# Optimization experiments

Hardware: AMD Instinct MI355X
Metric: run time of the kernel (lower is better)

Reference implementation:

```python
import jax, jax.numpy as jnp
import numpy as np

N_NODES = 50000
N_EDGES = 800000
HIDDEN = 128
BN_EPS = 1e-5
LEAKY_SLOPE = 0.01


def setup_inputs() -> dict:
    key = jax.random.key(0)
    ks = jax.random.split(key, 8)
    x = jax.random.normal(ks[0], (N_NODES, HIDDEN), dtype=jnp.float32)
    edge_index = jax.random.randint(ks[1], (2, N_EDGES), 0, N_NODES, dtype=jnp.int64)
    # stacked per-layer params (4 SAGEConv layers, all 128->128)
    sc = 1.0 / np.sqrt(HIDDEN)
    Wl = jax.random.normal(ks[2], (4, HIDDEN, HIDDEN), dtype=jnp.float32) * sc
    bl = jax.random.normal(ks[3], (4, HIDDEN), dtype=jnp.float32) * sc
    Wr = jax.random.normal(ks[4], (4, HIDDEN, HIDDEN), dtype=jnp.float32) * sc
    gamma = jnp.ones((4, HIDDEN), dtype=jnp.float32)
    beta = jnp.zeros((4, HIDDEN), dtype=jnp.float32)
    return {"x": x, "edge_index": edge_index, "Wl": Wl, "bl": bl,
            "Wr": Wr, "gamma": gamma, "beta": beta}


def _sage_mean_agg(x, src, dst, n):
    # gather source features per edge, scatter-mean onto destination nodes
    msg = x[src]                                                  # [E, F]
    agg = jax.ops.segment_sum(msg, dst, num_segments=n)           # [N, F]
    cnt = jax.ops.segment_sum(jnp.ones_like(dst, dtype=x.dtype), dst, num_segments=n)
    return agg / jnp.maximum(cnt, 1.0)[:, None]


def _bn_train(x, g, b):
    mu = jnp.mean(x, axis=0)
    var = jnp.mean((x - mu) ** 2, axis=0)  # biased variance (PyTorch BN normalization)
    return (x - mu) * jax.lax.rsqrt(var + BN_EPS) * g + b


def reference(x, edge_index, Wl, bl, Wr, gamma, beta):
    src, dst = edge_index[0], edge_index[1]
    n = x.shape[0]
    h = x
    for i in range(4):
        agg = _sage_mean_agg(h, src, dst, n)
        h = agg @ Wl[i] + bl[i] + h @ Wr[i]          # SAGEConv: lin_l(mean_nbr) + lin_r(root)
        h = jnp.where(h >= 0, h, LEAKY_SLOPE * h)    # leaky_relu
        h = _bn_train(h, gamma[i], beta[i])
    # dropout: eval-mode identity (deterministic reference)
    return h
```

## Files before the change

### kernel.cpp

```cpp
#include <hip/hip_runtime.h>
#include <hip/hip_bf16.h>

#define N_NODES 50000
#define N_EDGES 800000
#define F 128
#define BN_EPS 1e-5f
#define SLOPE 0.01f
#define NB 782
#define CAP 64
#define NBIN 128
#define BINSZ 391
#define QCAP2 8192
#define ABLK 512
#define AITER 7
#define PB1 6250
#define PB2 512

typedef __attribute__((ext_vector_type(8))) __bf16 bf16x8_t;
typedef __attribute__((ext_vector_type(8))) unsigned short u16x8_t;
typedef __attribute__((ext_vector_type(4))) float f32x4_t;

__device__ __forceinline__ unsigned short f2b(float f) {
    unsigned int u = __float_as_uint(f);
    unsigned int r = (u + 0x7fffu + ((u >> 16) & 1u)) >> 16;
    return (unsigned short)r;
}
__device__ __forceinline__ float b2f_lo(unsigned int v) { return __uint_as_float(v << 16); }
__device__ __forceinline__ float b2f_hi(unsigned int v) { return __uint_as_float(v & 0xffff0000u); }


__global__ __launch_bounds__(256) void bucket2_kernel(const int* __restrict__ src,
                                                      const int* __restrict__ dst,
                                                      int* __restrict__ qtail,
                                                      unsigned int* __restrict__ qdata) {
    __shared__ int counts[NBIN];
    __shared__ int cur[NBIN];
    __shared__ int base[NBIN];
    const int tid = threadIdx.x;

    for (int k = tid; k < NBIN; k += 256) { counts[k] = 0; cur[k] = 0; }
    __syncthreads();

    unsigned int pack[AITER];
    int bin[AITER];
    const int stride = ABLK * 256;
#pragma unroll
    for (int it = 0; it < AITER; ++it) {
        const int e = blockIdx.x * 256 + tid + it * stride;
        bin[it] = -1;
        if (e < N_EDGES) {
            int d = __builtin_nontemporal_load(dst + e);
            int s = __builtin_nontemporal_load(src + e);
            bin[it] = d / BINSZ;
            pack[it] = ((unsigned int)d << 16) | (unsigned int)s;
            atomicAdd(&counts[bin[it]], 1);
        }
    }
    __syncthreads();
    if (tid < NBIN) {
        int c = counts[tid];
        base[tid] = (c > 0) ? atomicAdd(&qtail[tid * 16], c) : 0;
    }
    __syncthreads();
#pragma unroll
    for (int it = 0; it < AITER; ++it) {
        if (bin[it] >= 0) {
            int slot = base[bin[it]] + atomicAdd(&cur[bin[it]], 1);
            qdata[(long)bin[it] * QCAP2 + slot] = pack[it];
        }
    }
}

__global__ __launch_bounds__(256) void scatter2_kernel(const unsigned int* __restrict__ qdata,
                                                       const int* __restrict__ qtail,
                                                       int* __restrict__ deg,
                                                       unsigned short* __restrict__ csr) {
    __shared__ int cnt[BINSZ];
    __shared__ unsigned short stage[BINSZ][CAP];
    const int b = blockIdx.x;
    const int nbase = b * BINSZ;
    const int nn = min(BINSZ, N_NODES - nbase);
    const int tid = threadIdx.x;

    for (int r = tid; r < BINSZ; r += 256) cnt[r] = 0;
    __syncthreads();

    const int n = qtail[b * 16];
    const unsigned int* q = qdata + (long)b * QCAP2;
    for (int i = tid; i < n; i += 256) {
        unsigned int p = q[i];
        int local = (int)(p >> 16) - nbase;
        int pos = atomicAdd(&cnt[local], 1);
        if (pos < CAP) stage[local][pos] = (unsigned short)(p & 0xffff);
    }
    __syncthreads();

    for (int c = tid; c < nn * (CAP / 8); c += 256) {
        const int r = c >> 3;
        const int col = (c & 7) * 8;
        *(u16x8_t*)(csr + (long)(nbase + r) * CAP + col) = *(const u16x8_t*)&stage[r][col];
    }
    for (int r = tid; r < nn; r += 256) deg[nbase + r] = min(cnt[r], CAP);
}


__global__ __launch_bounds__(256) void prep_kernel(const float* __restrict__ x,
                                                   unsigned short* __restrict__ hb,
                                                   const float* __restrict__ Wl,
                                                   const float* __restrict__ Wr,
                                                   unsigned short* __restrict__ Wt,
                                                   float* __restrict__ scale,
                                                   float* __restrict__ shift) {
    const int b = blockIdx.x;
    const int tid = threadIdx.x;
    if (b < PB1) {
        long i = (long)b * 256 + tid;
        float4 v = ((const float4*)x)[i];
        ushort4 o;
        o.x = f2b(v.x); o.y = f2b(v.y); o.z = f2b(v.z); o.w = f2b(v.w);
        ((ushort4*)hb)[i] = o;
    } else if (b < PB1 + PB2) {
        int idx = (b - PB1) * 256 + tid;
        int k = idx & 255;
        int n = (idx >> 8) & 127;
        int i = idx >> 15;
        float v = (k < F) ? Wl[((long)i * F + k) * F + n]
                          : Wr[((long)i * F + (k - F)) * F + n];
        Wt[idx] = f2b(v);
    } else {
        if (tid < F) { scale[tid] = 1.f; shift[tid] = 0.f; }
    }
}


__global__ __launch_bounds__(256) void agg_kernel(const unsigned short* __restrict__ h,
                                                  const int* __restrict__ deg,
                                                  const unsigned short* __restrict__ csr,
                                                  const float* __restrict__ scale,
                                                  const float* __restrict__ shift,
                                                  unsigned short* __restrict__ agg) {
    int node = (int)((blockIdx.x * (unsigned)blockDim.x + threadIdx.x) >> 6);
    int lane = threadIdx.x & 63;
    if (node >= N_NODES) return;
    const int g = lane >> 4;
    const int fl = lane & 15;
    const int d = deg[node];
    const int beg = node * CAP;
    const unsigned short* hl = h + fl * 8;

    float a0 = 0.f, a1 = 0.f, a2 = 0.f, a3 = 0.f;
    float a4 = 0.f, a5 = 0.f, a6 = 0.f, a7 = 0.f;

    for (int e0 = 0; e0 < d; e0 += 16) {
        int idx[4];
#pragma unroll
        for (int s = 0; s < 4; ++s) {
            const int ee = e0 + s * 4 + g;
            idx[s] = (int)csr[beg + ((ee < d) ? ee : 0)];
        }
        uint4 v[4];
#pragma unroll
        for (int s = 0; s < 4; ++s)
            v[s] = *(const uint4*)(hl + (long)idx[s] * F);
#pragma unroll
        for (int s = 0; s < 4; ++s) {
            const bool ok = (e0 + s * 4 + g) < d;
            const unsigned int w0 = ok ? v[s].x : 0u;
            const unsigned int w1 = ok ? v[s].y : 0u;
            const unsigned int w2 = ok ? v[s].z : 0u;
            const unsigned int w3 = ok ? v[s].w : 0u;
            a0 += b2f_lo(w0); a1 += b2f_hi(w0);
            a2 += b2f_lo(w1); a3 += b2f_hi(w1);
            a4 += b2f_lo(w2); a5 += b2f_hi(w2);
            a6 += b2f_lo(w3); a7 += b2f_hi(w3);
        }
    }

    a0 += __shfl_xor(a0, 16); a1 += __shfl_xor(a1, 16);
    a2 += __shfl_xor(a2, 16); a3 += __shfl_xor(a3, 16);
    a4 += __shfl_xor(a4, 16); a5 += __shfl_xor(a5, 16);
    a6 += __shfl_xor(a6, 16); a7 += __shfl_xor(a7, 16);
    a0 += __shfl_xor(a0, 32); a1 += __shfl_xor(a1, 32);
    a2 += __shfl_xor(a2, 32); a3 += __shfl_xor(a3, 32);
    a4 += __shfl_xor(a4, 32); a5 += __shfl_xor(a5, 32);
    a6 += __shfl_xor(a6, 32); a7 += __shfl_xor(a7, 32);

    u16x8_t o;
    if (d > 0) {
        const float inv = 1.0f / (float)d;
        const float4 sc0 = ((const float4*)scale)[fl * 2];
        const float4 sc1 = ((const float4*)scale)[fl * 2 + 1];
        const float4 sh0 = ((const float4*)shift)[fl * 2];
        const float4 sh1 = ((const float4*)shift)[fl * 2 + 1];
        o[0] = f2b(a0 * inv * sc0.x + sh0.x);
        o[1] = f2b(a1 * inv * sc0.y + sh0.y);
        o[2] = f2b(a2 * inv * sc0.z + sh0.z);
        o[3] = f2b(a3 * inv * sc0.w + sh0.w);
        o[4] = f2b(a4 * inv * sc1.x + sh1.x);
        o[5] = f2b(a5 * inv * sc1.y + sh1.y);
        o[6] = f2b(a6 * inv * sc1.z + sh1.z);
        o[7] = f2b(a7 * inv * sc1.w + sh1.w);
    } else {
#pragma unroll
        for (int j = 0; j < 8; ++j) o[j] = 0;
    }
    if (lane < 16)
        *(u16x8_t*)(agg + (long)node * F + lane * 8) = o;
}

__device__ __forceinline__ u16x8_t affine8(u16x8_t av, const float* __restrict__ sc,
                                           const float* __restrict__ sh) {
    u16x8_t r;
#pragma unroll
    for (int j = 0; j < 8; ++j) {
        float v = __uint_as_float(((unsigned int)av[j]) << 16);
        v = v * sc[j] + sh[j];
        r[j] = f2b(v);
    }
    return r;
}

__global__ __launch_bounds__(256) void gemm_mfma(const unsigned short* __restrict__ aggb,
                                                 const unsigned short* __restrict__ hin,
                                                 const float* __restrict__ scale,
                                                 const float* __restrict__ shift,
                                                 const unsigned short* __restrict__ Wt,
                                                 const float* __restrict__ bl,
                                                 unsigned short* __restrict__ Pb,
                                                 float* __restrict__ partial) {
    __shared__ __align__(16) char shraw[32768];
    unsigned short* stage = (unsigned short*)shraw;
    unsigned short* ep16 = (unsigned short*)shraw;
    __shared__ float lsum[4][F];
    __shared__ float lsq[4][F];

    const int tid = threadIdx.x;
    const int wave = tid >> 6, lane = tid & 63;
    const int m = lane & 15, q = lane >> 4;
    const int rbase = blockIdx.x * 64 + wave * 16;
    const int arow = rbase + m;
    const bool aval = arow < N_NODES;
    const unsigned short* ap = aggb + (long)arow * F + q * 8;
    const unsigned short* hp = hin + (long)arow * F + q * 8;

    u16x8_t areg[8];
#pragma unroll
    for (int j = 0; j < 8; ++j) areg[j] = (u16x8_t)0;
    if (aval) {
#pragma unroll
        for (int j = 0; j < 4; ++j) areg[j] = *(const u16x8_t*)(ap + j * 32);
#pragma unroll
        for (int j = 0; j < 4; ++j) {
            u16x8_t raw = *(const u16x8_t*)(hp + j * 32);
            const int base = j * 32 + q * 8;
            areg[4 + j] = affine8(raw, scale + base, shift + base);
        }
    }

    f32x4_t acc[8];
#pragma unroll
    for (int nt = 0; nt < 8; ++nt) acc[nt] = (f32x4_t){0.f, 0.f, 0.f, 0.f};

    for (int half = 0; half < 2; ++half) {
        if (half) __syncthreads();
#pragma unroll
        for (int f = 0; f < 8; ++f) {
            const int fid = f * 256 + tid;
            const int lf = fid & 63;
            const int ksf = (fid >> 6) & 3;
            const int ntf = fid >> 8;
            const int n = ntf * 16 + (lf & 15);
            const int k = half * 128 + ksf * 32 + (lf >> 4) * 8;
            const unsigned short* gsrc = Wt + (long)n * 256 + k;
#if __has_builtin(__builtin_amdgcn_global_load_lds)
            unsigned short* lbase = stage + (f * 256 + wave * 64) * 8;
            __builtin_amdgcn_global_load_lds(
                (const __attribute__((address_space(1))) void*)gsrc,
                (__attribute__((address_space(3))) void*)lbase, 16, 0, 0);
#else
            *(u16x8_t*)(stage + fid * 8) = *(const u16x8_t*)gsrc;
#endif
        }
        __syncthreads();
#pragma unroll
        for (int ks = 0; ks < 4; ++ks) {
            bf16x8_t af = __builtin_bit_cast(bf16x8_t, areg[half * 4 + ks]);
#pragma unroll
            for (int nt = 0; nt < 8; ++nt) {
                u16x8_t bv = *(const u16x8_t*)(stage + ((nt * 4 + ks) * 64 + lane) * 8);
                bf16x8_t bf = __builtin_bit_cast(bf16x8_t, bv);
                acc[nt] = __builtin_amdgcn_mfma_f32_16x16x32_bf16(af, bf, acc[nt], 0, 0, 0);
            }
        }
    }

    __syncthreads();

    float cs[8], cq[8];
#pragma unroll
    for (int nt = 0; nt < 8; ++nt) {
        cs[nt] = 0.f; cq[nt] = 0.f;
        const int c = nt * 16 + m;
        const float b = bl[c];
#pragma unroll
        for (int r = 0; r < 4; ++r) {
            const int rl = wave * 16 + q * 4 + r;
            float v = acc[nt][r] + b;
            v = (v >= 0.f) ? v : SLOPE * v;
            ep16[rl * 136 + c] = f2b(v);
            if (rbase + q * 4 + r < N_NODES) {
                cs[nt] += v;
                cq[nt] += v * v;
            }
        }
    }

    {
        const int rq = lane >> 4;
        const int cc = (lane & 15) * 8;
#pragma unroll
        for (int r2 = 0; r2 < 4; ++r2) {
            const int rl = wave * 16 + rq * 4 + r2;
            const int grow = blockIdx.x * 64 + rl;
            if (grow < N_NODES)
                *(u16x8_t*)(Pb + (long)grow * F + cc) = *(const u16x8_t*)(ep16 + rl * 136 + cc);
        }
    }

#pragma unroll
    for (int nt = 0; nt < 8; ++nt) {
        cs[nt] += __shfl_xor(cs[nt], 16);
        cs[nt] += __shfl_xor(cs[nt], 32);
        cq[nt] += __shfl_xor(cq[nt], 16);
        cq[nt] += __shfl_xor(cq[nt], 32);
    }
    if (lane < 16) {
#pragma unroll
        for (int nt = 0; nt < 8; ++nt) {
            lsum[wave][nt * 16 + m] = cs[nt];
            lsq[wave][nt * 16 + m] = cq[nt];
        }
    }
    __syncthreads();
    if (tid < F) {
        float s = 0.f, s2 = 0.f;
#pragma unroll
        for (int w = 0; w < 4; ++w) {
            s += lsum[w][tid];
            s2 += lsq[w][tid];
        }
        partial[(long)blockIdx.x * 256 + tid] = s;
        partial[(long)blockIdx.x * 256 + 128 + tid] = s2;
    }
}

__global__ __launch_bounds__(256) void bn_reduce(const float* __restrict__ partial,
                                                 const float* __restrict__ gamma,
                                                 const float* __restrict__ beta,
                                                 float* __restrict__ scale,
                                                 float* __restrict__ shift) {
    const int j = blockIdx.x;
    const int t = threadIdx.x;
    const int lane = t & 63, wave = t >> 6;
    float s = 0.f, s2 = 0.f;
    for (int b = t; b < NB; b += 256) {
        s += partial[(long)b * 256 + j];
        s2 += partial[(long)b * 256 + 128 + j];
    }
#pragma unroll
    for (int off = 1; off < 64; off <<= 1) {
        s += __shfl_xor(s, off);
        s2 += __shfl_xor(s2, off);
    }
    __shared__ float ls[4], lq[4];
    if (lane == 0) { ls[wave] = s; lq[wave] = s2; }
    __syncthreads();
    if (t == 0) {
        float S = ls[0] + ls[1] + ls[2] + ls[3];
        float Q = lq[0] + lq[1] + lq[2] + lq[3];
        const float inv_n = 1.0f / (float)N_NODES;
        float mu = S * inv_n;
        float var = Q * inv_n - mu * mu;
        float scl = gamma[j] * rsqrtf(var + BN_EPS);
        scale[j] = scl;
        shift[j] = beta[j] - mu * scl;
    }
}

__global__ __launch_bounds__(256) void bn_apply_f(const unsigned short* __restrict__ Pb,
                                                  float* __restrict__ out,
                                                  const float* __restrict__ scale,
                                                  const float* __restrict__ shift) {
    long i = (long)blockIdx.x * blockDim.x + threadIdx.x;
    if (i >= (long)N_NODES * (F / 8)) return;
    const int c8 = (int)(i & 15);
    uint4 v = ((const uint4*)Pb)[i];
    const float4 sc0 = ((const float4*)scale)[c8 * 2];
    const float4 sc1 = ((const float4*)scale)[c8 * 2 + 1];
    const float4 sh0 = ((const float4*)shift)[c8 * 2];
    const float4 sh1 = ((const float4*)shift)[c8 * 2 + 1];
    float4 o0, o1;
    o0.x = b2f_lo(v.x) * sc0.x + sh0.x;
    o0.y = b2f_hi(v.x) * sc0.y + sh0.y;
    o0.z = b2f_lo(v.y) * sc0.z + sh0.z;
    o0.w = b2f_hi(v.y) * sc0.w + sh0.w;
    o1.x = b2f_lo(v.z) * sc1.x + sh1.x;
    o1.y = b2f_hi(v.z) * sc1.y + sh1.y;
    o1.z = b2f_lo(v.w) * sc1.z + sh1.z;
    o1.w = b2f_hi(v.w) * sc1.w + sh1.w;
    ((float4*)out)[i * 2] = o0;
    ((float4*)out)[i * 2 + 1] = o1;
}


extern "C" void kernel_launch(void* const* d_in, const int* in_sizes, int n_in,
                              void* d_out, int out_size, void* d_ws, size_t ws_size,
                              hipStream_t stream) {
    const float* x     = (const float*)d_in[0];
    const int*   ei    = (const int*)d_in[1];
    const float* Wl    = (const float*)d_in[2];
    const float* bl    = (const float*)d_in[3];
    const float* Wr    = (const float*)d_in[4];
    const float* gamma = (const float*)d_in[5];
    const float* beta  = (const float*)d_in[6];
    float* out = (float*)d_out;

    const int* src = ei;
    const int* dst = ei + N_EDGES;

    char* w = (char*)d_ws;
    auto alloc = [&](size_t bytes) -> char* {
        char* p = w;
        w += (bytes + 255) & ~(size_t)255;
        return p;
    };
    unsigned short* hbA   = (unsigned short*)alloc((size_t)N_NODES * F * 2);
    unsigned short* hbB   = (unsigned short*)alloc((size_t)N_NODES * F * 2);
    unsigned short* aggb  = (unsigned short*)alloc((size_t)N_NODES * F * 2);
    unsigned short* Wt    = (unsigned short*)alloc((size_t)4 * F * 256 * 2);
    int*   deg      = (int*)alloc((size_t)N_NODES * 4);
    int*   qtail    = (int*)alloc((size_t)NBIN * 16 * 4);
    unsigned int* qdata = (unsigned int*)alloc((size_t)NBIN * QCAP2 * 4);
    unsigned short* csr = (unsigned short*)alloc((size_t)N_NODES * CAP * 2);
    float* partial  = (float*)alloc((size_t)NB * 256 * 4);
    float* scale    = (float*)alloc(F * 4);
    float* shift    = (float*)alloc(F * 4);

    hipMemsetAsync(qtail, 0, (size_t)NBIN * 16 * 4, stream);

    bucket2_kernel<<<ABLK, 256, 0, stream>>>(src, dst, qtail, qdata);
    scatter2_kernel<<<NBIN, 256, 0, stream>>>(qdata, qtail, deg, csr);
    prep_kernel<<<PB1 + PB2 + 1, 256, 0, stream>>>(x, hbA, Wl, Wr, Wt, scale, shift);

    const int n8 = N_NODES * (F / 8);

    unsigned short* hin = hbA;
    unsigned short* hnext = hbB;
    for (int i = 0; i < 4; ++i) {
        agg_kernel<<<(N_NODES + 3) / 4, 256, 0, stream>>>(hin, deg, csr, scale, shift, aggb);

        gemm_mfma<<<NB, 256, 0, stream>>>(
            aggb, hin, scale, shift, Wt + (size_t)i * F * 256, bl + (size_t)i * F,
            hnext, partial);

        bn_reduce<<<F, 256, 0, stream>>>(partial, gamma + (size_t)i * F, beta + (size_t)i * F,
                                         scale, shift);

        unsigned short* t = hin; hin = hnext; hnext = t;
    }
    bn_apply_f<<<(n8 + 255) / 256, 256, 0, stream>>>(hin, out, scale, shift);
}
```

Before: 355.1 us.

## Fuse neighbor mean aggregation into the MFMA GEMM kernel

Removes the separate aggregation kernel and its bf16 agg buffer. The GEMM kernel now gathers neighbor rows itself, with each lane walking one node's CSR list and accumulating 32 features while the first weight half is staged into LDS. This saves a kernel launch and the write and read-back of the aggregate buffer in every layer. In exchange the gather becomes serial per node with only 782 blocks of 4 waves, so there is much less memory-level parallelism and the serial per-edge index chain may leave gather latency exposed.

After: 400.2 us. 12.7% more time.

```diff
diff --git a/kernel.cpp b/kernel.cpp
--- a/kernel.cpp
+++ b/kernel.cpp
@@ -133,101 +133,80 @@
 }
 
 
-__global__ __launch_bounds__(256) void agg_kernel(const unsigned short* __restrict__ h,
+__device__ __forceinline__ u16x8_t affine8(u16x8_t av, const float* __restrict__ sc,
+                                           const float* __restrict__ sh) {
+    u16x8_t r;
+#pragma unroll
+    for (int j = 0; j < 8; ++j) {
+        float v = __uint_as_float(((unsigned int)av[j]) << 16);
+        v = v * sc[j] + sh[j];
+        r[j] = f2b(v);
+    }
+    return r;
+}
+
+#define ACC8(A, V)                               \
+    A[0] += b2f_lo(V.x); A[1] += b2f_hi(V.x);    \
+    A[2] += b2f_lo(V.y); A[3] += b2f_hi(V.y);    \
+    A[4] += b2f_lo(V.z); A[5] += b2f_hi(V.z);    \
+    A[6] += b2f_lo(V.w); A[7] += b2f_hi(V.w);
+
+#define PACKJ(j, A) {                                                   \
+    const float4 s0 = *(const float4*)(scale + q * 8 + 32 * (j));       \
+    const float4 s1 = *(const float4*)(scale + q * 8 + 32 * (j) + 4);   \
+    const float4 t0 = *(const float4*)(shift + q * 8 + 32 * (j));       \
+    const float4 t1 = *(const float4*)(shift + q * 8 + 32 * (j) + 4);   \
+    u16x8_t r;                                                          \
+    r[0] = f2b(A[0] * inv * s0.x + t0.x);                               \
+    r[1] = f2b(A[1] * inv * s0.y + t0.y);                               \
+    r[2] = f2b(A[2] * inv * s0.z + t0.z);                               \
+    r[3] = f2b(A[3] * inv * s0.w + t0.w);                               \
+    r[4] = f2b(A[4] * inv * s1.x + t1.x);                               \
+    r[5] = f2b(A[5] * inv * s1.y + t1.y);                               \
+    r[6] = f2b(A[6] * inv * s1.z + t1.z);                               \
+    r[7] = f2b(A[7] * inv * s1.w + t1.w);                               \
+    areg[j] = r; }
+
+#if __has_builtin(__builtin_amdgcn_global_load_lds)
+#define STAGE_HALF(half) {                                                        \
+    _Pragma("unroll")                                                             \
+    for (int f = 0; f < 8; ++f) {                                                 \
+        const int fid = f * 256 + tid;                                            \
+        const int lf = fid & 63;                                                  \
+        const int ksf = (fid >> 6) & 3;                                           \
+        const int ntf = fid >> 8;                                                 \
+        const int n = ntf * 16 + (lf & 15);                                       \
+        const int k = (half) * 128 + ksf * 32 + (lf >> 4) * 8;                    \
+        const unsigned short* gsrc = Wt + (long)n * 256 + k;                      \
+        unsigned short* lbase = stage + (f * 256 + wave * 64) * 8;                \
+        __builtin_amdgcn_global_load_lds(                                         \
+            (const __attribute__((address_space(1))) void*)gsrc,                  \
+            (__attribute__((address_space(3))) void*)lbase, 16, 0, 0);            \
+    } }
+#else
+#define STAGE_HALF(half) {                                                        \
+    _Pragma("unroll")                                                             \
+    for (int f = 0; f < 8; ++f) {                                                 \
+        const int fid = f * 256 + tid;                                            \
+        const int lf = fid & 63;                                                  \
+        const int ksf = (fid >> 6) & 3;                                           \
+        const int ntf = fid >> 8;                                                 \
+        const int n = ntf * 16 + (lf & 15);                                       \
+        const int k = (half) * 128 + ksf * 32 + (lf >> 4) * 8;                    \
+        const unsigned short* gsrc = Wt + (long)n * 256 + k;                      \
+        *(u16x8_t*)(stage + fid * 8) = *(const u16x8_t*)gsrc;                     \
+    } }
+#endif
+
+__global__ __launch_bounds__(256) void gemm_fused(const unsigned short* __restrict__ hin,
                                                   const int* __restrict__ deg,
                                                   const unsigned short* __restrict__ csr,
                                                   const float* __restrict__ scale,
                                                   const float* __restrict__ shift,
-                                                  unsigned short* __restrict__ agg) {
-    int node = (int)((blockIdx.x * (unsigned)blockDim.x + threadIdx.x) >> 6);
-    int lane = threadIdx.x & 63;
-    if (node >= N_NODES) return;
-    const int g = lane >> 4;
-    const int fl = lane & 15;
-    const int d = deg[node];
-    const int beg = node * CAP;
-    const unsigned short* hl = h + fl * 8;
-
-    float a0 = 0.f, a1 = 0.f, a2 = 0.f, a3 = 0.f;
-    float a4 = 0.f, a5 = 0.f, a6 = 0.f, a7 = 0.f;
-
-    for (int e0 = 0; e0 < d; e0 += 16) {
-        int idx[4];
-#pragma unroll
-        for (int s = 0; s < 4; ++s) {
-            const int ee = e0 + s * 4 + g;
-            idx[s] = (int)csr[beg + ((ee < d) ? ee : 0)];
-        }
-        uint4 v[4];
-#pragma unroll
-        for (int s = 0; s < 4; ++s)
-            v[s] = *(const uint4*)(hl + (long)idx[s] * F);
-#pragma unroll
-        for (int s = 0; s < 4; ++s) {
-            const bool ok = (e0 + s * 4 + g) < d;
-            const unsigned int w0 = ok ? v[s].x : 0u;
-            const unsigned int w1 = ok ? v[s].y : 0u;
-            const unsigned int w2 = ok ? v[s].z : 0u;
-            const unsigned int w3 = ok ? v[s].w : 0u;
-            a0 += b2f_lo(w0); a1 += b2f_hi(w0);
-            a2 += b2f_lo(w1); a3 += b2f_hi(w1);
-            a4 += b2f_lo(w2); a5 += b2f_hi(w2);
-            a6 += b2f_lo(w3); a7 += b2f_hi(w3);
-        }
-    }
-
-    a0 += __shfl_xor(a0, 16); a1 += __shfl_xor(a1, 16);
-    a2 += __shfl_xor(a2, 16); a3 += __shfl_xor(a3, 16);
-    a4 += __shfl_xor(a4, 16); a5 += __shfl_xor(a5, 16);
-    a6 += __shfl_xor(a6, 16); a7 += __shfl_xor(a7, 16);
-    a0 += __shfl_xor(a0, 32); a1 += __shfl_xor(a1, 32);
-    a2 += __shfl_xor(a2, 32); a3 += __shfl_xor(a3, 32);
-    a4 += __shfl_xor(a4, 32); a5 += __shfl_xor(a5, 32);
-    a6 += __shfl_xor(a6, 32); a7 += __shfl_xor(a7, 32);
-
-    u16x8_t o;
-    if (d > 0) {
-        const float inv = 1.0f / (float)d;
-        const float4 sc0 = ((const float4*)scale)[fl * 2];
-        const float4 sc1 = ((const float4*)scale)[fl * 2 + 1];
-        const float4 sh0 = ((const float4*)shift)[fl * 2];
-        const float4 sh1 = ((const float4*)shift)[fl * 2 + 1];
-        o[0] = f2b(a0 * inv * sc0.x + sh0.x);
-        o[1] = f2b(a1 * inv * sc0.y + sh0.y);
-        o[2] = f2b(a2 * inv * sc0.z + sh0.z);
-        o[3] = f2b(a3 * inv * sc0.w + sh0.w);
-        o[4] = f2b(a4 * inv * sc1.x + sh1.x);
-        o[5] = f2b(a5 * inv * sc1.y + sh1.y);
-        o[6] = f2b(a6 * inv * sc1.z + sh1.z);
-        o[7] = f2b(a7 * inv * sc1.w + sh1.w);
-    } else {
-#pragma unroll
-        for (int j = 0; j < 8; ++j) o[j] = 0;
-    }
-    if (lane < 16)
-        *(u16x8_t*)(agg + (long)node * F + lane * 8) = o;
-}
-
-__device__ __forceinline__ u16x8_t affine8(u16x8_t av, const float* __restrict__ sc,
-                                           const float* __restrict__ sh) {
-    u16x8_t r;
-#pragma unroll
-    for (int j = 0; j < 8; ++j) {
-        float v = __uint_as_float(((unsigned int)av[j]) << 16);
-        v = v * sc[j] + sh[j];
-        r[j] = f2b(v);
-    }
-    return r;
-}
-
-__global__ __launch_bounds__(256) void gemm_mfma(const unsigned short* __restrict__ aggb,
-                                                 const unsigned short* __restrict__ hin,
-                                                 const float* __restrict__ scale,
-                                                 const float* __restrict__ shift,
-                                                 const unsigned short* __restrict__ Wt,
-                                                 const float* __restrict__ bl,
-                                                 unsigned short* __restrict__ Pb,
-                                                 float* __restrict__ partial) {
+                                                  const unsigned short* __restrict__ Wt,
+                                                  const float* __restrict__ bl,
+                                                  unsigned short* __restrict__ Pb,
+                                                  float* __restrict__ partial) {
     __shared__ __align__(16) char shraw[32768];
     unsigned short* stage = (unsigned short*)shraw;
     unsigned short* ep16 = (unsigned short*)shraw;
@@ -240,20 +219,55 @@
     const int rbase = blockIdx.x * 64 + wave * 16;
     const int arow = rbase + m;
     const bool aval = arow < N_NODES;
-    const unsigned short* ap = aggb + (long)arow * F + q * 8;
+
+    STAGE_HALF(0);
+
     const unsigned short* hp = hin + (long)arow * F + q * 8;
+    u16x8_t hraw[4];
+#pragma unroll
+    for (int j = 0; j < 4; ++j) hraw[j] = (u16x8_t)0;
+    if (aval) {
+#pragma unroll
+        for (int j = 0; j < 4; ++j) hraw[j] = *(const u16x8_t*)(hp + j * 32);
+    }
+
+    const int d = aval ? deg[arow] : 0;
+    const unsigned short* crow = csr + (long)arow * CAP;
+    const unsigned short* hq = hin + q * 8;
+    float a0[8], a1[8], a2[8], a3[8];
+#pragma unroll
+    for (int j = 0; j < 8; ++j) { a0[j] = 0.f; a1[j] = 0.f; a2[j] = 0.f; a3[j] = 0.f; }
+
+    int snext = (d > 0) ? (int)crow[0] : 0;
+    for (int e = 0; e < d; ++e) {
+        const int s = snext;
+        if (e + 1 < d) snext = (int)crow[e + 1];
+        const unsigned short* hr = hq + (long)s * F;
+        uint4 v0 = *(const uint4*)(hr);
+        uint4 v1 = *(const uint4*)(hr + 32);
+        uint4 v2 = *(const uint4*)(hr + 64);
+        uint4 v3 = *(const uint4*)(hr + 96);
+        ACC8(a0, v0);
+        ACC8(a1, v1);
+        ACC8(a2, v2);
+        ACC8(a3, v3);
+    }
 
     u16x8_t areg[8];
 #pragma unroll
     for (int j = 0; j < 8; ++j) areg[j] = (u16x8_t)0;
+    if (d > 0) {
+        const float inv = 1.0f / (float)d;
+        PACKJ(0, a0);
+        PACKJ(1, a1);
+        PACKJ(2, a2);
+        PACKJ(3, a3);
+    }
     if (aval) {
 #pragma unroll
-        for (int j = 0; j < 4; ++j) areg[j] = *(const u16x8_t*)(ap + j * 32);
-#pragma unroll
         for (int j = 0; j < 4; ++j) {
-            u16x8_t raw = *(const u16x8_t*)(hp + j * 32);
             const int base = j * 32 + q * 8;
-            areg[4 + j] = affine8(raw, scale + base, shift + base);
+            areg[4 + j] = affine8(hraw[j], scale + base, shift + base);
         }
     }
 
@@ -261,36 +275,28 @@
 #pragma unroll
     for (int nt = 0; nt < 8; ++nt) acc[nt] = (f32x4_t){0.f, 0.f, 0.f, 0.f};
 
-    for (int half = 0; half < 2; ++half) {
-        if (half) __syncthreads();
-#pragma unroll
-        for (int f = 0; f < 8; ++f) {
-            const int fid = f * 256 + tid;
-            const int lf = fid & 63;
-            const int ksf = (fid >> 6) & 3;
-            const int ntf = fid >> 8;
-            const int n = ntf * 16 + (lf & 15);
-            const int k = half * 128 + ksf * 32 + (lf >> 4) * 8;
-            const unsigned short* gsrc = Wt + (long)n * 256 + k;
-#if __has_builtin(__builtin_amdgcn_global_load_lds)
-            unsigned short* lbase = stage + (f * 256 + wave * 64) * 8;
-            __builtin_amdgcn_global_load_lds(
-                (const __attribute__((address_space(1))) void*)gsrc,
-                (__attribute__((address_space(3))) void*)lbase, 16, 0, 0);
-#else
-            *(u16x8_t*)(stage + fid * 8) = *(const u16x8_t*)gsrc;
-#endif
-        }
-        __syncthreads();
-#pragma unroll
-        for (int ks = 0; ks < 4; ++ks) {
-            bf16x8_t af = __builtin_bit_cast(bf16x8_t, areg[half * 4 + ks]);
-#pragma unroll
-            for (int nt = 0; nt < 8; ++nt) {
-                u16x8_t bv = *(const u16x8_t*)(stage + ((nt * 4 + ks) * 64 + lane) * 8);
-                bf16x8_t bf = __builtin_bit_cast(bf16x8_t, bv);
-                acc[nt] = __builtin_amdgcn_mfma_f32_16x16x32_bf16(af, bf, acc[nt], 0, 0, 0);
-            }
+    __syncthreads();
+#pragma unroll
+    for (int ks = 0; ks < 4; ++ks) {
+        bf16x8_t af = __builtin_bit_cast(bf16x8_t, areg[ks]);
+#pragma unroll
+        for (int nt = 0; nt < 8; ++nt) {
+            u16x8_t bv = *(const u16x8_t*)(stage + ((nt * 4 + ks) * 64 + lane) * 8);
+            bf16x8_t bf = __builtin_bit_cast(bf16x8_t, bv);
+            acc[nt] = __builtin_amdgcn_mfma_f32_16x16x32_bf16(af, bf, acc[nt], 0, 0, 0);
+        }
+    }
+    __syncthreads();
+    STAGE_HALF(1);
+    __syncthreads();
+#pragma unroll
+    for (int ks = 0; ks < 4; ++ks) {
+        bf16x8_t af = __builtin_bit_cast(bf16x8_t, areg[4 + ks]);
+#pragma unroll
+        for (int nt = 0; nt < 8; ++nt) {
+            u16x8_t bv = *(const u16x8_t*)(stage + ((nt * 4 + ks) * 64 + lane) * 8);
+            bf16x8_t bf = __builtin_bit_cast(bf16x8_t, bv);
+            acc[nt] = __builtin_amdgcn_mfma_f32_16x16x32_bf16(af, bf, acc[nt], 0, 0, 0);
         }
     }
 
@@ -436,7 +442,6 @@
     };
     unsigned short* hbA   = (unsigned short*)alloc((size_t)N_NODES * F * 2);
     unsigned short* hbB   = (unsigned short*)alloc((size_t)N_NODES * F * 2);
-    unsigned short* aggb  = (unsigned short*)alloc((size_t)N_NODES * F * 2);
     unsigned short* Wt    = (unsigned short*)alloc((size_t)4 * F * 256 * 2);
     int*   deg      = (int*)alloc((size_t)N_NODES * 4);
     int*   qtail    = (int*)alloc((size_t)NBIN * 16 * 4);
@@ -457,10 +462,8 @@
     unsigned short* hin = hbA;
     unsigned short* hnext = hbB;
     for (int i = 0; i < 4; ++i) {
-        agg_kernel<<<(N_NODES + 3) / 4, 256, 0, stream>>>(hin, deg, csr, scale, shift, aggb);
-
-        gemm_mfma<<<NB, 256, 0, stream>>>(
-            aggb, hin, scale, shift, Wt + (size_t)i * F * 256, bl + (size_t)i * F,
+        gemm_fused<<<NB, 256, 0, stream>>>(
+            hin, deg, csr, scale, shift, Wt + (size_t)i * F * 256, bl + (size_t)i * F,
             hnext, partial);
 
         bn_reduce<<<F, 256, 0, stream>>>(partial, gamma + (size_t)i * F, beta + (size_t)i * F,
```
